# Optimization experiments

Measured on AMD Instinct MI355X. Metric: run time of the kernel, lower is better.

Reference implementation:

```python
import jax, jax.numpy as jnp
import numpy as np

THRESH = 0.5
MARGIN = 0.1
SCALE_POS = 2.0
SCALE_NEG = 50.0
EPS = 1e-5


def setup_inputs() -> dict:
    key = jax.random.key(0)
    k1, k2 = jax.random.split(key)
    B, D = 8192, 256
    feats = jax.random.normal(k1, (B, D), dtype=jnp.float32)
    # speaker embeddings are L2-normalized (cosine similarity, thresh=0.5 assumes this)
    feats = feats / jnp.linalg.norm(feats, axis=-1, keepdims=True)
    labels = jax.random.randint(k2, (B,), 0, 512, dtype=jnp.int64)
    return {"feats": feats, "labels": labels}


def reference(feats, labels):
    B = feats.shape[0]
    sim = jnp.matmul(feats, feats.T)                      # [B, B]
    same = labels[:, None] == labels[None, :]             # [B, B]

    pos_mask = same & (sim < 1.0 - EPS)                   # pos_pair_ (drops self-sim ~1)
    neg_mask = ~same                                      # neg_pair_

    neg_inf = jnp.float32(-jnp.inf)
    pos_inf = jnp.float32(jnp.inf)
    min_pos = jnp.min(jnp.where(pos_mask, sim, pos_inf), axis=1)  # min(pos_pair_)
    max_neg = jnp.max(jnp.where(neg_mask, sim, neg_inf), axis=1)  # max(neg_pair_)

    # dynamic re-masking (hard mining)
    neg_sel = neg_mask & (sim > (min_pos - MARGIN)[:, None])
    pos_sel = pos_mask & (sim < (max_neg + MARGIN)[:, None])

    valid = jnp.any(neg_sel, axis=1) & jnp.any(pos_sel, axis=1)

    # masked sums of exponentials via exp(-inf)=0; single fused mask+exp+sum
    pos_sum = jnp.sum(jnp.exp(jnp.where(pos_sel, -SCALE_POS * (sim - THRESH), neg_inf)), axis=1)
    neg_sum = jnp.sum(jnp.exp(jnp.where(neg_sel, SCALE_NEG * (sim - THRESH), neg_inf)), axis=1)

    row_loss = (1.0 / SCALE_POS) * jnp.log1p(pos_sum) + (1.0 / SCALE_NEG) * jnp.log1p(neg_sum)
    loss = jnp.sum(jnp.where(valid, row_loss, 0.0)) / B
    prec1 = jnp.mean(1.0 - valid.astype(jnp.float32))
    return loss, prec1
```

## Files before the change

kernel.cpp:

```cpp
#include <hip/hip_runtime.h>
#include <hip/hip_cooperative_groups.h>
#include <stdint.h>

namespace cg = cooperative_groups;


typedef __attribute__((ext_vector_type(8))) short short8;
typedef __attribute__((ext_vector_type(4))) float floatx4;

constexpr int D = 256;
constexpr int BM = 128;
constexpr int NT = 64;
constexpr int GPS = 8;
constexpr int NPB = NT * GPS;
constexpr int CPS = 33;
constexpr int BT = 512;
constexpr int CHUNK_SH = BM * 64;

__device__ __forceinline__ unsigned f2bf(float f) {
  unsigned u = __float_as_uint(f);
  return (u + 0x7FFFu + ((u >> 16) & 1u)) >> 16;
}

__device__ __forceinline__ void gl_lds16(const void* g, void* l) {
  __builtin_amdgcn_global_load_lds(
      (const __attribute__((address_space(1))) unsigned int*)g,
      (__attribute__((address_space(3))) unsigned int*)l, 16, 0, 0);
}

template <int PASS>
__device__ __forceinline__ void pair_body(
    int bid, const unsigned short* __restrict__ fb, const int* __restrict__ labels,
    const float* __restrict__ tmn, const float* __restrict__ tmx,
    float* __restrict__ rp0, float* __restrict__ rp1,
    float* __restrict__ cp0, float* __restrict__ cp1,
    short* As, short* Bs, int* labA, float* tA0, float* tA1) {
  const int I   = bid >> 3;
  const int g   = bid & 7;
  const int nT  = (I < 32) ? 33 : 32;
  const int t0  = (g * nT) >> 3;
  const int t1  = ((g + 1) * nT) >> 3;
  const int row0 = I * BM;

  const int tid  = threadIdx.x;
  const int lane = tid & 63;
  const int wave = tid >> 6;
  const int l15  = lane & 15;
  const int quad = lane >> 4;
  const int wr   = (wave >> 1) * 32;
  const int wc   = (wave & 1) * 64;

  const float ONE_EPS = 1.0f - 1e-5f;
  const float INF = __builtin_inff();

  __syncthreads();
  if (tid < BM) {
    labA[tid] = labels[row0 + tid];
    if (PASS == 2) { tA0[tid] = tmn[row0 + tid]; tA1[tid] = tmx[row0 + tid]; }
  }

  auto stage = [&](int b, int col0, int kc) {
#pragma unroll
    for (int j = 0; j < 2; ++j) {
      int idx = j * BT + tid;
      int r   = idx >> 3;
      int sl  = idx & 7;
      int cb  = sl ^ (r & 7);
      const char* ga = (const char*)fb + (((size_t)(row0 + r)) << 9) + (kc << 7) + (cb << 4);
      const char* gb = (const char*)fb + (((size_t)(col0 + r)) << 9) + (kc << 7) + (cb << 4);
      gl_lds16(ga, (char*)As + (size_t)b * (CHUNK_SH * 2) + ((size_t)idx << 4));
      gl_lds16(gb, (char*)Bs + (size_t)b * (CHUNK_SH * 2) + ((size_t)idx << 4));
    }
  };

  int arow[2], brow[4];
#pragma unroll
  for (int i = 0; i < 2; ++i) arow[i] = wr + i * 16 + l15;
#pragma unroll
  for (int i = 0; i < 4; ++i) brow[i] = wc + i * 16 + l15;

  float s0[8], s1[8];
#pragma unroll
  for (int i = 0; i < 8; ++i) {
    s0[i] = (PASS == 1) ? INF : 0.f;
    s1[i] = (PASS == 1) ? -INF : 0.f;
  }

  stage(0, ((I + t0) & 63) * BM, 0);

  int cur = 0;
  for (int off = t0; off < t1; ++off) {
    const int J = (I + off) & 63;
    const int col0 = J * BM;
    const bool diag = (off == 0);

    floatx4 acc[2][4];
#pragma unroll
    for (int rf = 0; rf < 2; ++rf)
#pragma unroll
      for (int cf = 0; cf < 4; ++cf)
        acc[rf][cf] = (floatx4)(0.f);

#pragma unroll
    for (int kc = 0; kc < 4; ++kc) {
      if (kc < 3) {
        stage(cur ^ 1, col0, kc + 1);
        asm volatile("s_waitcnt vmcnt(4)" ::: "memory");
      } else if (off + 1 < t1) {
        stage(cur ^ 1, ((I + off + 1) & 63) * BM, 0);
        asm volatile("s_waitcnt vmcnt(4)" ::: "memory");
      } else {
        asm volatile("s_waitcnt vmcnt(0)" ::: "memory");
      }
      __builtin_amdgcn_s_barrier();
      asm volatile("" ::: "memory");

      const short* Ab = As + cur * CHUNK_SH;
      const short* Bb = Bs + cur * CHUNK_SH;
#pragma unroll
      for (int ks = 0; ks < 2; ++ks) {
        const int gg = ks * 4 + quad;
        short8 a[2], b[4];
#pragma unroll
        for (int rf = 0; rf < 2; ++rf)
          a[rf] = *(const short8*)(Ab + arow[rf] * 64 + ((gg ^ (arow[rf] & 7)) << 3));
#pragma unroll
        for (int cf = 0; cf < 4; ++cf)
          b[cf] = *(const short8*)(Bb + brow[cf] * 64 + ((gg ^ (brow[cf] & 7)) << 3));
#pragma unroll
        for (int rf = 0; rf < 2; ++rf)
#pragma unroll
          for (int cf = 0; cf < 4; ++cf)
            acc[rf][cf] = __builtin_amdgcn_mfma_f32_16x16x32_bf16(a[rf], b[cf], acc[rf][cf], 0, 0, 0);
      }
      asm volatile("s_waitcnt lgkmcnt(0)" ::: "memory");
      __builtin_amdgcn_s_barrier();
      asm volatile("" ::: "memory");
      cur ^= 1;
    }

    int labc[4];
    float tBn[4], tBx[4];
#pragma unroll
    for (int cf = 0; cf < 4; ++cf) {
      int ci = col0 + wc + cf * 16 + l15;
      labc[cf] = labels[ci];
      if (PASS == 2) { tBn[cf] = tmn[ci]; tBx[cf] = tmx[ci]; }
    }

    float c0[4], c1[4];
#pragma unroll
    for (int i = 0; i < 4; ++i) {
      c0[i] = (PASS == 1) ? INF : 0.f;
      c1[i] = (PASS == 1) ? -INF : 0.f;
    }

#pragma unroll
    for (int rf = 0; rf < 2; ++rf) {
#pragma unroll
      for (int r = 0; r < 4; ++r) {
        const int ri = wr + rf * 16 + quad * 4 + r;
        const int lr = labA[ri];
        float tRn = 0.f, tRx = 0.f;
        if (PASS == 2) { tRn = tA0[ri]; tRx = tA1[ri]; }
#pragma unroll
        for (int cf = 0; cf < 4; ++cf) {
          float sim = acc[rf][cf][r];
          bool same = (lr == labc[cf]);
          bool posok = same && (sim < ONE_EPS);
          if (PASS == 1) {
            float pc = posok ? sim : INF;
            float nc = same ? -INF : sim;
            s0[rf * 4 + r] = fminf(s0[rf * 4 + r], pc);
            s1[rf * 4 + r] = fmaxf(s1[rf * 4 + r], nc);
            c0[cf] = fminf(c0[cf], pc);
            c1[cf] = fmaxf(c1[cf], nc);
          } else {
            if (posok) {
              float e = __expf(fmaf(-2.f, sim, 1.f));
              if (sim < tRx)      s0[rf * 4 + r] += e;
              if (sim < tBx[cf])  c0[cf] += e;
            } else if (!same) {
              float e = (sim > 0.22f) ? __expf(fmaf(50.f, sim, -25.f)) : 0.f;
              if (sim > tRn)      s1[rf * 4 + r] += 1e-30f + e;
              if (sim > tBn[cf])  c1[cf] += 1e-30f + e;
            }
          }
        }
      }
    }

    if (!diag) {
#pragma unroll
      for (int cf = 0; cf < 4; ++cf) {
        float v = c0[cf], w = c1[cf];
#pragma unroll
        for (int m = 16; m < 64; m <<= 1) {
          float vv = __shfl_xor(v, m), ww = __shfl_xor(w, m);
          v = (PASS == 1) ? fminf(v, vv) : (v + vv);
          w = (PASS == 1) ? fmaxf(w, ww) : (w + ww);
        }
        if (quad == 0) {
          size_t o = (size_t)(I * CPS + off) * 512 + (size_t)(wr >> 5) * 128 + wc + cf * 16 + l15;
          cp0[o] = v;
          cp1[o] = w;
        }
      }
    }
  }

#pragma unroll
  for (int i = 0; i < 8; ++i) {
#pragma unroll
    for (int m = 1; m < 16; m <<= 1) {
      float v = __shfl_xor(s0[i], m), w = __shfl_xor(s1[i], m);
      s0[i] = (PASS == 1) ? fminf(s0[i], v) : (s0[i] + v);
      s1[i] = (PASS == 1) ? fmaxf(s1[i], w) : (s1[i] + w);
    }
  }
  if (l15 == 0) {
#pragma unroll
    for (int rf = 0; rf < 2; ++rf)
#pragma unroll
      for (int r = 0; r < 4; ++r) {
        int ri = wr + rf * 16 + quad * 4 + r;
        size_t o = (size_t)bid * 256 + (size_t)(wc >> 6) * 128 + ri;
        rp0[o] = s0[rf * 4 + r];
        rp1[o] = s1[rf * 4 + r];
      }
  }
}

template <int PASS>
__device__ __forceinline__ void reduce_body(
    int T, const float* __restrict__ rp0, const float* __restrict__ rp1,
    const float* __restrict__ cp0, const float* __restrict__ cp1,
    float* __restrict__ o0, float* __restrict__ o1, float* __restrict__ out,
    float* sA, float* sB, float* sred) {
  const int q  = threadIdx.x & 127;
  const int h4 = threadIdx.x >> 7;

  float a = (PASS == 1) ? __builtin_inff() : 0.f;
  float b = (PASS == 1) ? -__builtin_inff() : 0.f;
#pragma unroll
  for (int g = 0; g < 4; ++g) {
    int c = h4 * 4 + g;
    int gg = c >> 1, half = c & 1;
    size_t o = (size_t)(T * GPS + gg) * 256 + (size_t)half * 128 + q;
    float v0 = rp0[o], v1 = rp1[o];
    a = (PASS == 1) ? fminf(a, v0) : (a + v0);
    b = (PASS == 1) ? fmaxf(b, v1) : (b + v1);
  }
#pragma unroll
  for (int off = 1; off <= 31; ++off) {
    int Is = (T - off) & 63;
    size_t o = (size_t)(Is * CPS + off) * 512 + (size_t)h4 * 128 + q;
    float v0 = cp0[o], v1 = cp1[o];
    a = (PASS == 1) ? fminf(a, v0) : (a + v0);
    b = (PASS == 1) ? fmaxf(b, v1) : (b + v1);
  }
  if (T >= 32) {
    int Is = T - 32;
    size_t o = (size_t)(Is * CPS + 32) * 512 + (size_t)h4 * 128 + q;
    float v0 = cp0[o], v1 = cp1[o];
    a = (PASS == 1) ? fminf(a, v0) : (a + v0);
    b = (PASS == 1) ? fmaxf(b, v1) : (b + v1);
  }
  if (h4 > 0) { sA[(h4 - 1) * 128 + q] = a; sB[(h4 - 1) * 128 + q] = b; }
  __syncthreads();
  if (h4 == 0) {
#pragma unroll
    for (int p = 0; p < 3; ++p) {
      float v0 = sA[p * 128 + q], v1 = sB[p * 128 + q];
      a = (PASS == 1) ? fminf(a, v0) : (a + v0);
      b = (PASS == 1) ? fmaxf(b, v1) : (b + v1);
    }
    if (PASS == 1) {
      o0[T * 128 + q] = a - 0.1f;
      o1[T * 128 + q] = b + 0.1f;
    } else {
      float loss = 0.f, cnt = 0.f;
      if (a > 0.f && b > 0.f) {
        loss = 0.5f * log1pf(a) + 0.02f * log1pf(b);
        cnt = 1.f;
      }
#pragma unroll
      for (int m = 1; m < 64; m <<= 1) {
        loss += __shfl_xor(loss, m);
        cnt  += __shfl_xor(cnt, m);
      }
      int wv = threadIdx.x >> 6, ln = threadIdx.x & 63;
      if (ln == 0) { sred[wv] = loss; sred[4 + wv] = cnt; }
    }
  }
  if (PASS == 2) {
    __syncthreads();
    if (threadIdx.x == 0) {
      float L = sred[0] + sred[1];
      float C = sred[4] + sred[5];
      atomicAdd(out, L / 8192.0f);
      atomicAdd(out + 1, -C / 8192.0f);
    }
  }
}

__global__ __launch_bounds__(BT, 4)
void mega_kernel(const float* feats, const int* labels, unsigned short* fb,
                 float* rp0, float* rp1, float* cp0, float* cp1,
                 float* tmn, float* tmx, float* out) {
  __shared__ __align__(16) short As[2 * CHUNK_SH];
  __shared__ __align__(16) short Bs[2 * CHUNK_SH];
  __shared__ int   labA[BM];
  __shared__ float tA0[BM], tA1[BM];

  cg::grid_group grid = cg::this_grid();
  const int bid = blockIdx.x;
  const int tid = threadIdx.x;

  const int n4 = 8192 * D / 4;
  for (int i = bid * BT + tid; i < n4; i += NPB * BT) {
    float4 v = ((const float4*)feats)[i];
    unsigned lo = f2bf(v.x) | (f2bf(v.y) << 16);
    unsigned hi = f2bf(v.z) | (f2bf(v.w) << 16);
    ((uint2*)fb)[i] = make_uint2(lo, hi);
  }
  if (bid == 0 && tid == 0) { out[0] = 0.f; out[1] = 1.f; }
  __threadfence();
  grid.sync();

  pair_body<1>(bid, fb, labels, nullptr, nullptr, rp0, rp1, cp0, cp1,
               As, Bs, labA, tA0, tA1);
  __threadfence();
  grid.sync();

  if (bid < NT)
    reduce_body<1>(bid, rp0, rp1, cp0, cp1, tmn, tmx, out,
                   (float*)As, (float*)As + 384, (float*)As + 768);
  __threadfence();
  grid.sync();

  pair_body<2>(bid, fb, labels, tmn, tmx, rp0, rp1, cp0, cp1,
               As, Bs, labA, tA0, tA1);
  __threadfence();
  grid.sync();

  if (bid < NT)
    reduce_body<2>(bid, rp0, rp1, cp0, cp1, nullptr, nullptr, out,
                   (float*)As, (float*)As + 384, (float*)As + 768);
}

__global__ void convert_kernel(const float* __restrict__ feats,
                               unsigned short* __restrict__ fb, int n4,
                               float* __restrict__ out) {
  int i = blockIdx.x * blockDim.x + threadIdx.x;
  if (i < n4) {
    float4 v = ((const float4*)feats)[i];
    unsigned lo = f2bf(v.x) | (f2bf(v.y) << 16);
    unsigned hi = f2bf(v.z) | (f2bf(v.w) << 16);
    ((uint2*)fb)[i] = make_uint2(lo, hi);
  }
  if (blockIdx.x == 0 && threadIdx.x == 0) { out[0] = 0.f; out[1] = 1.f; }
}

template <int PASS>
__global__ __launch_bounds__(BT, 4)
void pair_kernel(const unsigned short* __restrict__ fb, const int* __restrict__ labels,
                 const float* __restrict__ tmn, const float* __restrict__ tmx,
                 float* __restrict__ rp0, float* __restrict__ rp1,
                 float* __restrict__ cp0, float* __restrict__ cp1) {
  __shared__ __align__(16) short As[2 * CHUNK_SH];
  __shared__ __align__(16) short Bs[2 * CHUNK_SH];
  __shared__ int   labA[BM];
  __shared__ float tA0[BM], tA1[BM];
  pair_body<PASS>(blockIdx.x, fb, labels, tmn, tmx, rp0, rp1, cp0, cp1,
                  As, Bs, labA, tA0, tA1);
}

template <int PASS>
__global__ void reduce_kernel(const float* __restrict__ rp0, const float* __restrict__ rp1,
                              const float* __restrict__ cp0, const float* __restrict__ cp1,
                              float* __restrict__ o0, float* __restrict__ o1,
                              float* __restrict__ out) {
  __shared__ float sA[384], sB[384], sred[8];
  reduce_body<PASS>(blockIdx.x, rp0, rp1, cp0, cp1, o0, o1, out, sA, sB, sred);
}

extern "C" void kernel_launch(void* const* d_in, const int* in_sizes, int n_in,
                              void* d_out, int out_size, void* d_ws, size_t ws_size,
                              hipStream_t stream) {
  const float* feats  = (const float*)d_in[0];
  const int*   labels = (const int*)d_in[1];
  const int Bn = in_sizes[1];
  float* out = (float*)d_out;

  unsigned short* fb = (unsigned short*)d_ws;
  float* rp0 = (float*)((char*)d_ws + (size_t)Bn * D * 2);
  float* rp1 = rp0 + (size_t)NPB * 256;
  float* cp0 = rp1 + (size_t)NPB * 256;
  float* cp1 = cp0 + (size_t)NT * CPS * 512;
  float* tmn = cp1 + (size_t)NT * CPS * 512;
  float* tmx = tmn + Bn;

  bool launched = false;
  int maxb = 0;
  hipError_t qe = hipOccupancyMaxActiveBlocksPerMultiprocessor(
      &maxb, (const void*)mega_kernel, BT, 0);
  if (qe == hipSuccess && maxb * 256 >= NPB) {
    void* args[] = {(void*)&feats, (void*)&labels, (void*)&fb,
                    (void*)&rp0, (void*)&rp1, (void*)&cp0, (void*)&cp1,
                    (void*)&tmn, (void*)&tmx, (void*)&out};
    hipError_t le = hipLaunchCooperativeKernel(
        (const void*)mega_kernel, dim3(NPB), dim3(BT), args, 0, stream);
    launched = (le == hipSuccess);
  }
  if (!launched) {
    int n4 = Bn * D / 4;
    convert_kernel<<<(n4 + 255) / 256, 256, 0, stream>>>(feats, fb, n4, out);
    pair_kernel<1><<<NPB, BT, 0, stream>>>(fb, labels, nullptr, nullptr, rp0, rp1, cp0, cp1);
    reduce_kernel<1><<<NT, BT, 0, stream>>>(rp0, rp1, cp0, cp1, tmn, tmx, out);
    pair_kernel<2><<<NPB, BT, 0, stream>>>(fb, labels, tmn, tmx, rp0, rp1, cp0, cp1);
    reduce_kernel<2><<<NT, BT, 0, stream>>>(rp0, rp1, cp0, cp1, nullptr, nullptr, out);
  }
}
```

Before: 145.0 us.

## Cache pass-1 similarity tiles in workspace and reload them in pass 2

When the workspace is large enough, pass 1 writes each fp32 similarity tile to global memory with nontemporal stores. Pass 2 reloads these tiles instead of restaging bf16 features and recomputing the MFMA GEMM. This removes the second matrix multiply but adds a large write and read of the full similarity matrix through HBM. The path is selected at launch based on workspace size.

```diff
diff --git a/kernel.cpp b/kernel.cpp
--- a/kernel.cpp
+++ b/kernel.cpp
@@ -16,6 +16,8 @@
 constexpr int CPS = 33;
 constexpr int BT = 512;
 constexpr int CHUNK_SH = BM * 64;
+constexpr int TILE_SLOTS = NT * CPS;
+constexpr size_t TILE_V4 = 8 * BT;
 
 __device__ __forceinline__ unsigned f2bf(float f) {
   unsigned u = __float_as_uint(f);
@@ -28,13 +30,16 @@
       (__attribute__((address_space(3))) unsigned int*)l, 16, 0, 0);
 }
 
-template <int PASS>
+template <int PASS, bool CACHED>
 __device__ __forceinline__ void pair_body(
     int bid, const unsigned short* __restrict__ fb, const int* __restrict__ labels,
     const float* __restrict__ tmn, const float* __restrict__ tmx,
     float* __restrict__ rp0, float* __restrict__ rp1,
     float* __restrict__ cp0, float* __restrict__ cp1,
+    floatx4* __restrict__ simsv,
     short* As, short* Bs, int* labA, float* tA0, float* tA1) {
+  constexpr bool COMPUTE = (PASS == 1) || !CACHED;
+
   const int I   = bid >> 3;
   const int g   = bid & 7;
   const int nT  = (I < 32) ? 33 : 32;
@@ -57,6 +62,9 @@
   if (tid < BM) {
     labA[tid] = labels[row0 + tid];
     if (PASS == 2) { tA0[tid] = tmn[row0 + tid]; tA1[tid] = tmx[row0 + tid]; }
+  }
+  if constexpr (!COMPUTE) {
+    __syncthreads();
   }
 
   auto stage = [&](int b, int col0, int kc) {
@@ -86,7 +94,9 @@
     s1[i] = (PASS == 1) ? -INF : 0.f;
   }
 
-  stage(0, ((I + t0) & 63) * BM, 0);
+  if constexpr (COMPUTE) {
+    stage(0, ((I + t0) & 63) * BM, 0);
+  }
 
   int cur = 0;
   for (int off = t0; off < t1; ++off) {
@@ -94,51 +104,6 @@
     const int col0 = J * BM;
     const bool diag = (off == 0);
 
-    floatx4 acc[2][4];
-#pragma unroll
-    for (int rf = 0; rf < 2; ++rf)
-#pragma unroll
-      for (int cf = 0; cf < 4; ++cf)
-        acc[rf][cf] = (floatx4)(0.f);
-
-#pragma unroll
-    for (int kc = 0; kc < 4; ++kc) {
-      if (kc < 3) {
-        stage(cur ^ 1, col0, kc + 1);
-        asm volatile("s_waitcnt vmcnt(4)" ::: "memory");
-      } else if (off + 1 < t1) {
-        stage(cur ^ 1, ((I + off + 1) & 63) * BM, 0);
-        asm volatile("s_waitcnt vmcnt(4)" ::: "memory");
-      } else {
-        asm volatile("s_waitcnt vmcnt(0)" ::: "memory");
-      }
-      __builtin_amdgcn_s_barrier();
-      asm volatile("" ::: "memory");
-
-      const short* Ab = As + cur * CHUNK_SH;
-      const short* Bb = Bs + cur * CHUNK_SH;
-#pragma unroll
-      for (int ks = 0; ks < 2; ++ks) {
-        const int gg = ks * 4 + quad;
-        short8 a[2], b[4];
-#pragma unroll
-        for (int rf = 0; rf < 2; ++rf)
-          a[rf] = *(const short8*)(Ab + arow[rf] * 64 + ((gg ^ (arow[rf] & 7)) << 3));
-#pragma unroll
-        for (int cf = 0; cf < 4; ++cf)
-          b[cf] = *(const short8*)(Bb + brow[cf] * 64 + ((gg ^ (brow[cf] & 7)) << 3));
-#pragma unroll
-        for (int rf = 0; rf < 2; ++rf)
-#pragma unroll
-          for (int cf = 0; cf < 4; ++cf)
-            acc[rf][cf] = __builtin_amdgcn_mfma_f32_16x16x32_bf16(a[rf], b[cf], acc[rf][cf], 0, 0, 0);
-      }
-      asm volatile("s_waitcnt lgkmcnt(0)" ::: "memory");
-      __builtin_amdgcn_s_barrier();
-      asm volatile("" ::: "memory");
-      cur ^= 1;
-    }
-
     int labc[4];
     float tBn[4], tBx[4];
 #pragma unroll
@@ -146,6 +111,69 @@
       int ci = col0 + wc + cf * 16 + l15;
       labc[cf] = labels[ci];
       if (PASS == 2) { tBn[cf] = tmn[ci]; tBx[cf] = tmx[ci]; }
+    }
+
+    floatx4 acc[2][4];
+    if constexpr (COMPUTE) {
+#pragma unroll
+      for (int rf = 0; rf < 2; ++rf)
+#pragma unroll
+        for (int cf = 0; cf < 4; ++cf)
+          acc[rf][cf] = (floatx4)(0.f);
+
+#pragma unroll
+      for (int kc = 0; kc < 4; ++kc) {
+        if (kc < 3) {
+          stage(cur ^ 1, col0, kc + 1);
+          asm volatile("s_waitcnt vmcnt(4)" ::: "memory");
+        } else if (off + 1 < t1) {
+          stage(cur ^ 1, ((I + off + 1) & 63) * BM, 0);
+          asm volatile("s_waitcnt vmcnt(4)" ::: "memory");
+        } else {
+          asm volatile("s_waitcnt vmcnt(0)" ::: "memory");
+        }
+        __builtin_amdgcn_s_barrier();
+        asm volatile("" ::: "memory");
+
+        const short* Ab = As + cur * CHUNK_SH;
+        const short* Bb = Bs + cur * CHUNK_SH;
+#pragma unroll
+        for (int ks = 0; ks < 2; ++ks) {
+          const int gg = ks * 4 + quad;
+          short8 a[2], b[4];
+#pragma unroll
+          for (int rf = 0; rf < 2; ++rf)
+            a[rf] = *(const short8*)(Ab + arow[rf] * 64 + ((gg ^ (arow[rf] & 7)) << 3));
+#pragma unroll
+          for (int cf = 0; cf < 4; ++cf)
+            b[cf] = *(const short8*)(Bb + brow[cf] * 64 + ((gg ^ (brow[cf] & 7)) << 3));
+#pragma unroll
+          for (int rf = 0; rf < 2; ++rf)
+#pragma unroll
+            for (int cf = 0; cf < 4; ++cf)
+              acc[rf][cf] = __builtin_amdgcn_mfma_f32_16x16x32_bf16(a[rf], b[cf], acc[rf][cf], 0, 0, 0);
+        }
+        asm volatile("s_waitcnt lgkmcnt(0)" ::: "memory");
+        __builtin_amdgcn_s_barrier();
+        asm volatile("" ::: "memory");
+        cur ^= 1;
+      }
+    } else {
+      const floatx4* tp = simsv + (size_t)(I * CPS + off) * TILE_V4;
+#pragma unroll
+      for (int rf = 0; rf < 2; ++rf)
+#pragma unroll
+        for (int cf = 0; cf < 4; ++cf)
+          acc[rf][cf] = __builtin_nontemporal_load(tp + (size_t)(rf * 4 + cf) * BT + tid);
+    }
+
+    if constexpr (PASS == 1 && CACHED) {
+      floatx4* tp = simsv + (size_t)(I * CPS + off) * TILE_V4;
+#pragma unroll
+      for (int rf = 0; rf < 2; ++rf)
+#pragma unroll
+        for (int cf = 0; cf < 4; ++cf)
+          __builtin_nontemporal_store(acc[rf][cf], tp + (size_t)(rf * 4 + cf) * BT + tid);
     }
 
     float c0[4], c1[4];
@@ -304,10 +332,11 @@
   }
 }
 
+template <int CACHED>
 __global__ __launch_bounds__(BT, 4)
 void mega_kernel(const float* feats, const int* labels, unsigned short* fb,
                  float* rp0, float* rp1, float* cp0, float* cp1,
-                 float* tmn, float* tmx, float* out) {
+                 float* tmn, float* tmx, floatx4* simsv, float* out) {
   __shared__ __align__(16) short As[2 * CHUNK_SH];
   __shared__ __align__(16) short Bs[2 * CHUNK_SH];
   __shared__ int   labA[BM];
@@ -328,8 +357,9 @@
   __threadfence();
   grid.sync();
 
-  pair_body<1>(bid, fb, labels, nullptr, nullptr, rp0, rp1, cp0, cp1,
-               As, Bs, labA, tA0, tA1);
+  pair_body<1, (bool)CACHED>(bid, fb, labels, nullptr, nullptr,
+                             rp0, rp1, cp0, cp1, simsv,
+                             As, Bs, labA, tA0, tA1);
   __threadfence();
   grid.sync();
 
@@ -339,8 +369,9 @@
   __threadfence();
   grid.sync();
 
-  pair_body<2>(bid, fb, labels, tmn, tmx, rp0, rp1, cp0, cp1,
-               As, Bs, labA, tA0, tA1);
+  pair_body<2, (bool)CACHED>(bid, fb, labels, tmn, tmx,
+                             rp0, rp1, cp0, cp1, simsv,
+                             As, Bs, labA, tA0, tA1);
   __threadfence();
   grid.sync();
 
@@ -372,8 +403,8 @@
   __shared__ __align__(16) short Bs[2 * CHUNK_SH];
   __shared__ int   labA[BM];
   __shared__ float tA0[BM], tA1[BM];
-  pair_body<PASS>(blockIdx.x, fb, labels, tmn, tmx, rp0, rp1, cp0, cp1,
-                  As, Bs, labA, tA0, tA1);
+  pair_body<PASS, false>(blockIdx.x, fb, labels, tmn, tmx, rp0, rp1, cp0, cp1,
+                         nullptr, As, Bs, labA, tA0, tA1);
 }
 
 template <int PASS>
@@ -393,24 +424,28 @@
   const int Bn = in_sizes[1];
   float* out = (float*)d_out;
 
-  unsigned short* fb = (unsigned short*)d_ws;
-  float* rp0 = (float*)((char*)d_ws + (size_t)Bn * D * 2);
-  float* rp1 = rp0 + (size_t)NPB * 256;
-  float* cp0 = rp1 + (size_t)NPB * 256;
-  float* cp1 = cp0 + (size_t)NT * CPS * 512;
-  float* tmn = cp1 + (size_t)NT * CPS * 512;
-  float* tmx = tmn + Bn;
+  char* base = (char*)d_ws;
+  unsigned short* fb = (unsigned short*)base;
+  size_t o = (size_t)Bn * D * 2;
+  float* rp0 = (float*)(base + o);  o += (size_t)NPB * 256 * 4;
+  float* rp1 = (float*)(base + o);  o += (size_t)NPB * 256 * 4;
+  float* cp0 = (float*)(base + o);  o += (size_t)NT * CPS * 512 * 4;
+  float* cp1 = (float*)(base + o);  o += (size_t)NT * CPS * 512 * 4;
+  float* tmn = (float*)(base + o);  o += (size_t)Bn * 4;
+  float* tmx = (float*)(base + o);  o += (size_t)Bn * 4;
+  floatx4* simsv = (floatx4*)(base + o);
+  size_t need = o + (size_t)TILE_SLOTS * TILE_V4 * 16;
+  const int cached = (ws_size >= need) ? 1 : 0;
 
   bool launched = false;
   int maxb = 0;
-  hipError_t qe = hipOccupancyMaxActiveBlocksPerMultiprocessor(
-      &maxb, (const void*)mega_kernel, BT, 0);
+  const void* kfn = cached ? (const void*)mega_kernel<1> : (const void*)mega_kernel<0>;
+  hipError_t qe = hipOccupancyMaxActiveBlocksPerMultiprocessor(&maxb, kfn, BT, 0);
   if (qe == hipSuccess && maxb * 256 >= NPB) {
     void* args[] = {(void*)&feats, (void*)&labels, (void*)&fb,
                     (void*)&rp0, (void*)&rp1, (void*)&cp0, (void*)&cp1,
-                    (void*)&tmn, (void*)&tmx, (void*)&out};
-    hipError_t le = hipLaunchCooperativeKernel(
-        (const void*)mega_kernel, dim3(NPB), dim3(BT), args, 0, stream);
+                    (void*)&tmn, (void*)&tmx, (void*)&simsv, (void*)&out};
+    hipError_t le = hipLaunchCooperativeKernel(kfn, dim3(NPB), dim3(BT), args, 0, stream);
     launched = (le == hipSuccess);
   }
   if (!launched) {
```

After: 140.4 us. 3.2% less time.

## Replace second similarity GEMM pass with sparse candidate-pair records and atomic apply

Applied to the files above, without the earlier changes.

The first pair pass now also writes out the sparse set of candidate pairs: positives, plus negatives whose similarity exceeds 0.22. Each record carries the pair's indices and similarity and goes into a fixed-capacity buffer per block. A cheap apply phase then uses the mined thresholds and atomics to add the exponentials into per-row accumulators. This removes the second full bf16 GEMM recompute. The validity test is rewritten to compare the row extrema directly with the thresholds, and a label histogram stands in for the epsilon per-negative term. The costs are a shared-memory atomic inside the hot epilogue, global atomics during apply, and a per-block cap of 2048 records that assumes candidate pairs are sparse; excess records would be silently dropped.

```diff
diff --git a/kernel.cpp b/kernel.cpp
--- a/kernel.cpp
+++ b/kernel.cpp
@@ -16,6 +16,7 @@
 constexpr int CPS = 33;
 constexpr int BT = 512;
 constexpr int CHUNK_SH = BM * 64;
+constexpr int RECCAP = 2048;
 
 __device__ __forceinline__ unsigned f2bf(float f) {
   unsigned u = __float_as_uint(f);
@@ -28,13 +29,12 @@
       (__attribute__((address_space(3))) unsigned int*)l, 16, 0, 0);
 }
 
-template <int PASS>
-__device__ __forceinline__ void pair_body(
+__device__ __forceinline__ void pair1_body(
     int bid, const unsigned short* __restrict__ fb, const int* __restrict__ labels,
-    const float* __restrict__ tmn, const float* __restrict__ tmx,
     float* __restrict__ rp0, float* __restrict__ rp1,
     float* __restrict__ cp0, float* __restrict__ cp1,
-    short* As, short* Bs, int* labA, float* tA0, float* tA1) {
+    uint2* __restrict__ recs, int* __restrict__ reccnt,
+    short* As, short* Bs, int* labA, int* emitCnt) {
   const int I   = bid >> 3;
   const int g   = bid & 7;
   const int nT  = (I < 32) ? 33 : 32;
@@ -53,11 +53,9 @@
   const float ONE_EPS = 1.0f - 1e-5f;
   const float INF = __builtin_inff();
 
+  if (tid == 0) *emitCnt = 0;
   __syncthreads();
-  if (tid < BM) {
-    labA[tid] = labels[row0 + tid];
-    if (PASS == 2) { tA0[tid] = tmn[row0 + tid]; tA1[tid] = tmx[row0 + tid]; }
-  }
+  if (tid < BM) labA[tid] = labels[row0 + tid];
 
   auto stage = [&](int b, int col0, int kc) {
 #pragma unroll
@@ -81,10 +79,7 @@
 
   float s0[8], s1[8];
 #pragma unroll
-  for (int i = 0; i < 8; ++i) {
-    s0[i] = (PASS == 1) ? INF : 0.f;
-    s1[i] = (PASS == 1) ? -INF : 0.f;
-  }
+  for (int i = 0; i < 8; ++i) { s0[i] = INF; s1[i] = -INF; }
 
   stage(0, ((I + t0) & 63) * BM, 0);
 
@@ -93,6 +88,14 @@
     const int J = (I + off) & 63;
     const int col0 = J * BM;
     const bool diag = (off == 0);
+
+    int labc[4], cidx[4];
+#pragma unroll
+    for (int cf = 0; cf < 4; ++cf) {
+      int ci = col0 + wc + cf * 16 + l15;
+      cidx[cf] = ci;
+      labc[cf] = labels[ci];
+    }
 
     floatx4 acc[2][4];
 #pragma unroll
@@ -139,21 +142,9 @@
       cur ^= 1;
     }
 
-    int labc[4];
-    float tBn[4], tBx[4];
-#pragma unroll
-    for (int cf = 0; cf < 4; ++cf) {
-      int ci = col0 + wc + cf * 16 + l15;
-      labc[cf] = labels[ci];
-      if (PASS == 2) { tBn[cf] = tmn[ci]; tBx[cf] = tmx[ci]; }
-    }
-
     float c0[4], c1[4];
 #pragma unroll
-    for (int i = 0; i < 4; ++i) {
-      c0[i] = (PASS == 1) ? INF : 0.f;
-      c1[i] = (PASS == 1) ? -INF : 0.f;
-    }
+    for (int i = 0; i < 4; ++i) { c0[i] = INF; c1[i] = -INF; }
 
 #pragma unroll
     for (int rf = 0; rf < 2; ++rf) {
@@ -161,30 +152,24 @@
       for (int r = 0; r < 4; ++r) {
         const int ri = wr + rf * 16 + quad * 4 + r;
         const int lr = labA[ri];
-        float tRn = 0.f, tRx = 0.f;
-        if (PASS == 2) { tRn = tA0[ri]; tRx = tA1[ri]; }
 #pragma unroll
         for (int cf = 0; cf < 4; ++cf) {
           float sim = acc[rf][cf][r];
           bool same = (lr == labc[cf]);
           bool posok = same && (sim < ONE_EPS);
-          if (PASS == 1) {
-            float pc = posok ? sim : INF;
-            float nc = same ? -INF : sim;
-            s0[rf * 4 + r] = fminf(s0[rf * 4 + r], pc);
-            s1[rf * 4 + r] = fmaxf(s1[rf * 4 + r], nc);
-            c0[cf] = fminf(c0[cf], pc);
-            c1[cf] = fmaxf(c1[cf], nc);
-          } else {
-            if (posok) {
-              float e = __expf(fmaf(-2.f, sim, 1.f));
-              if (sim < tRx)      s0[rf * 4 + r] += e;
-              if (sim < tBx[cf])  c0[cf] += e;
-            } else if (!same) {
-              float e = (sim > 0.22f) ? __expf(fmaf(50.f, sim, -25.f)) : 0.f;
-              if (sim > tRn)      s1[rf * 4 + r] += 1e-30f + e;
-              if (sim > tBn[cf])  c1[cf] += 1e-30f + e;
-            }
+          float pc = posok ? sim : INF;
+          float nc = same ? -INF : sim;
+          s0[rf * 4 + r] = fminf(s0[rf * 4 + r], pc);
+          s1[rf * 4 + r] = fmaxf(s1[rf * 4 + r], nc);
+          c0[cf] = fminf(c0[cf], pc);
+          c1[cf] = fmaxf(c1[cf], nc);
+          bool hotn = (!same) && (sim > 0.22f);
+          if (posok || hotn) {
+            unsigned key = (unsigned)(row0 + ri) | ((unsigned)cidx[cf] << 13) |
+                           (diag ? (1u << 26) : 0u) | (hotn ? (1u << 27) : 0u);
+            int slot = atomicAdd(emitCnt, 1);
+            if (slot < RECCAP)
+              recs[(size_t)bid * RECCAP + slot] = make_uint2(key, __float_as_uint(sim));
           }
         }
       }
@@ -197,8 +182,8 @@
 #pragma unroll
         for (int m = 16; m < 64; m <<= 1) {
           float vv = __shfl_xor(v, m), ww = __shfl_xor(w, m);
-          v = (PASS == 1) ? fminf(v, vv) : (v + vv);
-          w = (PASS == 1) ? fmaxf(w, ww) : (w + ww);
+          v = fminf(v, vv);
+          w = fmaxf(w, ww);
         }
         if (quad == 0) {
           size_t o = (size_t)(I * CPS + off) * 512 + (size_t)(wr >> 5) * 128 + wc + cf * 16 + l15;
@@ -214,8 +199,8 @@
 #pragma unroll
     for (int m = 1; m < 16; m <<= 1) {
       float v = __shfl_xor(s0[i], m), w = __shfl_xor(s1[i], m);
-      s0[i] = (PASS == 1) ? fminf(s0[i], v) : (s0[i] + v);
-      s1[i] = (PASS == 1) ? fmaxf(s1[i], w) : (s1[i] + w);
+      s0[i] = fminf(s0[i], v);
+      s1[i] = fmaxf(s1[i], w);
     }
   }
   if (l15 == 0) {
@@ -229,89 +214,126 @@
         rp1[o] = s1[rf * 4 + r];
       }
   }
-}
-
-template <int PASS>
-__device__ __forceinline__ void reduce_body(
+  __syncthreads();
+  if (tid == 0) reccnt[bid] = (*emitCnt < RECCAP) ? *emitCnt : RECCAP;
+}
+
+__device__ __forceinline__ void reduce1_body(
     int T, const float* __restrict__ rp0, const float* __restrict__ rp1,
     const float* __restrict__ cp0, const float* __restrict__ cp1,
-    float* __restrict__ o0, float* __restrict__ o1, float* __restrict__ out,
-    float* sA, float* sB, float* sred) {
+    float* __restrict__ o0, float* __restrict__ o1,
+    float* __restrict__ mpv, float* __restrict__ mnv,
+    float* sA, float* sB) {
   const int q  = threadIdx.x & 127;
   const int h4 = threadIdx.x >> 7;
 
-  float a = (PASS == 1) ? __builtin_inff() : 0.f;
-  float b = (PASS == 1) ? -__builtin_inff() : 0.f;
+  float a = __builtin_inff();
+  float b = -__builtin_inff();
 #pragma unroll
   for (int g = 0; g < 4; ++g) {
     int c = h4 * 4 + g;
     int gg = c >> 1, half = c & 1;
     size_t o = (size_t)(T * GPS + gg) * 256 + (size_t)half * 128 + q;
-    float v0 = rp0[o], v1 = rp1[o];
-    a = (PASS == 1) ? fminf(a, v0) : (a + v0);
-    b = (PASS == 1) ? fmaxf(b, v1) : (b + v1);
+    a = fminf(a, rp0[o]);
+    b = fmaxf(b, rp1[o]);
   }
 #pragma unroll
   for (int off = 1; off <= 31; ++off) {
     int Is = (T - off) & 63;
     size_t o = (size_t)(Is * CPS + off) * 512 + (size_t)h4 * 128 + q;
-    float v0 = cp0[o], v1 = cp1[o];
-    a = (PASS == 1) ? fminf(a, v0) : (a + v0);
-    b = (PASS == 1) ? fmaxf(b, v1) : (b + v1);
+    a = fminf(a, cp0[o]);
+    b = fmaxf(b, cp1[o]);
   }
   if (T >= 32) {
     int Is = T - 32;
     size_t o = (size_t)(Is * CPS + 32) * 512 + (size_t)h4 * 128 + q;
-    float v0 = cp0[o], v1 = cp1[o];
-    a = (PASS == 1) ? fminf(a, v0) : (a + v0);
-    b = (PASS == 1) ? fmaxf(b, v1) : (b + v1);
+    a = fminf(a, cp0[o]);
+    b = fmaxf(b, cp1[o]);
   }
   if (h4 > 0) { sA[(h4 - 1) * 128 + q] = a; sB[(h4 - 1) * 128 + q] = b; }
   __syncthreads();
   if (h4 == 0) {
 #pragma unroll
     for (int p = 0; p < 3; ++p) {
-      float v0 = sA[p * 128 + q], v1 = sB[p * 128 + q];
-      a = (PASS == 1) ? fminf(a, v0) : (a + v0);
-      b = (PASS == 1) ? fmaxf(b, v1) : (b + v1);
-    }
-    if (PASS == 1) {
-      o0[T * 128 + q] = a - 0.1f;
-      o1[T * 128 + q] = b + 0.1f;
+      a = fminf(a, sA[p * 128 + q]);
+      b = fmaxf(b, sB[p * 128 + q]);
+    }
+    o0[T * 128 + q]  = a - 0.1f;
+    o1[T * 128 + q]  = b + 0.1f;
+    mpv[T * 128 + q] = a;
+    mnv[T * 128 + q] = b;
+  }
+}
+
+__device__ __forceinline__ void apply_body(
+    int bid, const uint2* __restrict__ recs, const int* __restrict__ reccnt,
+    const float* __restrict__ tmn, const float* __restrict__ tmx,
+    float* __restrict__ pos_acc, float* __restrict__ neg_acc) {
+  const int cnt = reccnt[bid];
+  for (int k = threadIdx.x; k < cnt; k += BT) {
+    uint2 rec = recs[(size_t)bid * RECCAP + k];
+    int ri = rec.x & 8191;
+    int ci = (rec.x >> 13) & 8191;
+    bool dg = (rec.x >> 26) & 1;
+    bool ng = (rec.x >> 27) & 1;
+    float sim = __uint_as_float(rec.y);
+    if (!ng) {
+      float e = __expf(fmaf(-2.f, sim, 1.f));
+      if (sim < tmx[ri])        atomicAdd(&pos_acc[ri], e);
+      if (!dg && sim < tmx[ci]) atomicAdd(&pos_acc[ci], e);
     } else {
-      float loss = 0.f, cnt = 0.f;
-      if (a > 0.f && b > 0.f) {
-        loss = 0.5f * log1pf(a) + 0.02f * log1pf(b);
-        cnt = 1.f;
-      }
-#pragma unroll
-      for (int m = 1; m < 64; m <<= 1) {
-        loss += __shfl_xor(loss, m);
-        cnt  += __shfl_xor(cnt, m);
-      }
-      int wv = threadIdx.x >> 6, ln = threadIdx.x & 63;
-      if (ln == 0) { sred[wv] = loss; sred[4 + wv] = cnt; }
-    }
-  }
-  if (PASS == 2) {
-    __syncthreads();
-    if (threadIdx.x == 0) {
-      float L = sred[0] + sred[1];
-      float C = sred[4] + sred[5];
-      atomicAdd(out, L / 8192.0f);
-      atomicAdd(out + 1, -C / 8192.0f);
-    }
+      float e = __expf(fmaf(50.f, sim, -25.f));
+      if (sim > tmn[ri])        atomicAdd(&neg_acc[ri], e);
+      if (!dg && sim > tmn[ci]) atomicAdd(&neg_acc[ci], e);
+    }
+  }
+}
+
+__device__ __forceinline__ void final_body(
+    int T, const int* __restrict__ labels, const int* __restrict__ labcnt,
+    const float* __restrict__ pos_acc, const float* __restrict__ neg_acc,
+    const float* __restrict__ tmn, const float* __restrict__ tmx,
+    const float* __restrict__ mpv, const float* __restrict__ mnv,
+    float* __restrict__ out, float* sred) {
+  const int tid = threadIdx.x;
+  float loss = 0.f, cval = 0.f;
+  if (tid < 128) {
+    int r = T * 128 + tid;
+    float a = pos_acc[r];
+    float b = neg_acc[r] + (float)(8192 - labcnt[labels[r]]) * 1e-30f;
+    bool valid = (mnv[r] > tmn[r]) && (mpv[r] < tmx[r]);
+    if (valid) {
+      loss = 0.5f * log1pf(a) + 0.02f * log1pf(b);
+      cval = 1.f;
+    }
+  }
+#pragma unroll
+  for (int m = 1; m < 64; m <<= 1) {
+    loss += __shfl_xor(loss, m);
+    cval += __shfl_xor(cval, m);
+  }
+  int wv = tid >> 6, ln = tid & 63;
+  if (ln == 0) { sred[wv] = loss; sred[8 + wv] = cval; }
+  __syncthreads();
+  if (tid == 0) {
+    float L = 0.f, C = 0.f;
+#pragma unroll
+    for (int w = 0; w < 8; ++w) { L += sred[w]; C += sred[8 + w]; }
+    atomicAdd(out, L / 8192.0f);
+    atomicAdd(out + 1, -C / 8192.0f);
   }
 }
 
 __global__ __launch_bounds__(BT, 4)
 void mega_kernel(const float* feats, const int* labels, unsigned short* fb,
                  float* rp0, float* rp1, float* cp0, float* cp1,
-                 float* tmn, float* tmx, float* out) {
+                 float* tmn, float* tmx, float* mpv, float* mnv,
+                 float* pos_acc, float* neg_acc, int* labcnt,
+                 uint2* recs, int* reccnt, float* out) {
   __shared__ __align__(16) short As[2 * CHUNK_SH];
   __shared__ __align__(16) short Bs[2 * CHUNK_SH];
-  __shared__ int   labA[BM];
-  __shared__ float tA0[BM], tA1[BM];
+  __shared__ int labA[BM];
+  __shared__ int emitCnt;
 
   cg::grid_group grid = cg::this_grid();
   const int bid = blockIdx.x;
@@ -324,34 +346,42 @@
     unsigned hi = f2bf(v.z) | (f2bf(v.w) << 16);
     ((uint2*)fb)[i] = make_uint2(lo, hi);
   }
+  for (int i = bid * BT + tid; i < 8192; i += NPB * BT) {
+    pos_acc[i] = 0.f;
+    neg_acc[i] = 0.f;
+  }
+  if (bid == 0 && tid < 512) labcnt[tid] = 0;
   if (bid == 0 && tid == 0) { out[0] = 0.f; out[1] = 1.f; }
   __threadfence();
   grid.sync();
 
-  pair_body<1>(bid, fb, labels, nullptr, nullptr, rp0, rp1, cp0, cp1,
-               As, Bs, labA, tA0, tA1);
+  pair1_body(bid, fb, labels, rp0, rp1, cp0, cp1, recs, reccnt,
+             As, Bs, labA, &emitCnt);
   __threadfence();
   grid.sync();
 
-  if (bid < NT)
-    reduce_body<1>(bid, rp0, rp1, cp0, cp1, tmn, tmx, out,
-                   (float*)As, (float*)As + 384, (float*)As + 768);
+  if (bid < NT) {
+    reduce1_body(bid, rp0, rp1, cp0, cp1, tmn, tmx, mpv, mnv,
+                 (float*)As, (float*)As + 384);
+  } else if (bid < NT + 16) {
+    for (int i = (bid - NT) * BT + tid; i < 8192; i += 16 * BT)
+      atomicAdd(&labcnt[labels[i]], 1);
+  }
   __threadfence();
   grid.sync();
 
-  pair_body<2>(bid, fb, labels, tmn, tmx, rp0, rp1, cp0, cp1,
-               As, Bs, labA, tA0, tA1);
+  apply_body(bid, recs, reccnt, tmn, tmx, pos_acc, neg_acc);
   __threadfence();
   grid.sync();
 
   if (bid < NT)
-    reduce_body<2>(bid, rp0, rp1, cp0, cp1, nullptr, nullptr, out,
-                   (float*)As, (float*)As + 384, (float*)As + 768);
-}
-
-__global__ void convert_kernel(const float* __restrict__ feats,
-                               unsigned short* __restrict__ fb, int n4,
-                               float* __restrict__ out) {
+    final_body(bid, labels, labcnt, pos_acc, neg_acc, tmn, tmx, mpv, mnv,
+               out, (float*)As);
+}
+
+__global__ void k_convert(const float* __restrict__ feats, unsigned short* __restrict__ fb,
+                          float* __restrict__ pos_acc, float* __restrict__ neg_acc,
+                          int* __restrict__ labcnt, float* __restrict__ out, int n4) {
   int i = blockIdx.x * blockDim.x + threadIdx.x;
   if (i < n4) {
     float4 v = ((const float4*)feats)[i];
@@ -359,30 +389,51 @@
     unsigned hi = f2bf(v.z) | (f2bf(v.w) << 16);
     ((uint2*)fb)[i] = make_uint2(lo, hi);
   }
-  if (blockIdx.x == 0 && threadIdx.x == 0) { out[0] = 0.f; out[1] = 1.f; }
-}
-
-template <int PASS>
+  if (i < 8192) { pos_acc[i] = 0.f; neg_acc[i] = 0.f; }
+  if (i < 512) labcnt[i] = 0;
+  if (i == 0) { out[0] = 0.f; out[1] = 1.f; }
+}
+
 __global__ __launch_bounds__(BT, 4)
-void pair_kernel(const unsigned short* __restrict__ fb, const int* __restrict__ labels,
-                 const float* __restrict__ tmn, const float* __restrict__ tmx,
-                 float* __restrict__ rp0, float* __restrict__ rp1,
-                 float* __restrict__ cp0, float* __restrict__ cp1) {
+void k_pair1(const unsigned short* __restrict__ fb, const int* __restrict__ labels,
+             float* __restrict__ rp0, float* __restrict__ rp1,
+             float* __restrict__ cp0, float* __restrict__ cp1,
+             uint2* __restrict__ recs, int* __restrict__ reccnt) {
   __shared__ __align__(16) short As[2 * CHUNK_SH];
   __shared__ __align__(16) short Bs[2 * CHUNK_SH];
-  __shared__ int   labA[BM];
-  __shared__ float tA0[BM], tA1[BM];
-  pair_body<PASS>(blockIdx.x, fb, labels, tmn, tmx, rp0, rp1, cp0, cp1,
-                  As, Bs, labA, tA0, tA1);
-}
-
-template <int PASS>
-__global__ void reduce_kernel(const float* __restrict__ rp0, const float* __restrict__ rp1,
-                              const float* __restrict__ cp0, const float* __restrict__ cp1,
-                              float* __restrict__ o0, float* __restrict__ o1,
-                              float* __restrict__ out) {
-  __shared__ float sA[384], sB[384], sred[8];
-  reduce_body<PASS>(blockIdx.x, rp0, rp1, cp0, cp1, o0, o1, out, sA, sB, sred);
+  __shared__ int labA[BM];
+  __shared__ int emitCnt;
+  pair1_body(blockIdx.x, fb, labels, rp0, rp1, cp0, cp1, recs, reccnt,
+             As, Bs, labA, &emitCnt);
+}
+
+__global__ void k_reduce1(const float* __restrict__ rp0, const float* __restrict__ rp1,
+                          const float* __restrict__ cp0, const float* __restrict__ cp1,
+                          float* __restrict__ tmn, float* __restrict__ tmx,
+                          float* __restrict__ mpv, float* __restrict__ mnv) {
+  __shared__ float sA[384], sB[384];
+  reduce1_body(blockIdx.x, rp0, rp1, cp0, cp1, tmn, tmx, mpv, mnv, sA, sB);
+}
+
+__global__ void k_hist(const int* __restrict__ labels, int* __restrict__ labcnt) {
+  int i = blockIdx.x * blockDim.x + threadIdx.x;
+  if (i < 8192) atomicAdd(&labcnt[labels[i]], 1);
+}
+
+__global__ void k_apply(const uint2* __restrict__ recs, const int* __restrict__ reccnt,
+                        const float* __restrict__ tmn, const float* __restrict__ tmx,
+                        float* __restrict__ pos_acc, float* __restrict__ neg_acc) {
+  apply_body(blockIdx.x, recs, reccnt, tmn, tmx, pos_acc, neg_acc);
+}
+
+__global__ void k_final(const int* __restrict__ labels, const int* __restrict__ labcnt,
+                        const float* __restrict__ pos_acc, const float* __restrict__ neg_acc,
+                        const float* __restrict__ tmn, const float* __restrict__ tmx,
+                        const float* __restrict__ mpv, const float* __restrict__ mnv,
+                        float* __restrict__ out) {
+  __shared__ float sred[16];
+  final_body(blockIdx.x, labels, labcnt, pos_acc, neg_acc, tmn, tmx, mpv, mnv,
+             out, sred);
 }
 
 extern "C" void kernel_launch(void* const* d_in, const int* in_sizes, int n_in,
@@ -393,13 +444,22 @@
   const int Bn = in_sizes[1];
   float* out = (float*)d_out;
 
-  unsigned short* fb = (unsigned short*)d_ws;
-  float* rp0 = (float*)((char*)d_ws + (size_t)Bn * D * 2);
-  float* rp1 = rp0 + (size_t)NPB * 256;
-  float* cp0 = rp1 + (size_t)NPB * 256;
-  float* cp1 = cp0 + (size_t)NT * CPS * 512;
-  float* tmn = cp1 + (size_t)NT * CPS * 512;
-  float* tmx = tmn + Bn;
+  char* base = (char*)d_ws;
+  unsigned short* fb = (unsigned short*)base;
+  size_t o = (size_t)Bn * D * 2;
+  float* rp0 = (float*)(base + o);  o += (size_t)NPB * 256 * 4;
+  float* rp1 = (float*)(base + o);  o += (size_t)NPB * 256 * 4;
+  float* cp0 = (float*)(base + o);  o += (size_t)NT * CPS * 512 * 4;
+  float* cp1 = (float*)(base + o);  o += (size_t)NT * CPS * 512 * 4;
+  uint2* recs = (uint2*)(base + o); o += (size_t)NPB * RECCAP * 8;
+  float* tmn = (float*)(base + o);  o += (size_t)Bn * 4;
+  float* tmx = (float*)(base + o);  o += (size_t)Bn * 4;
+  float* mpv = (float*)(base + o);  o += (size_t)Bn * 4;
+  float* mnv = (float*)(base + o);  o += (size_t)Bn * 4;
+  float* pos_acc = (float*)(base + o); o += (size_t)Bn * 4;
+  float* neg_acc = (float*)(base + o); o += (size_t)Bn * 4;
+  int* labcnt = (int*)(base + o);   o += 512 * 4;
+  int* reccnt = (int*)(base + o);   o += (size_t)NPB * 4;
 
   bool launched = false;
   int maxb = 0;
@@ -408,17 +468,20 @@
   if (qe == hipSuccess && maxb * 256 >= NPB) {
     void* args[] = {(void*)&feats, (void*)&labels, (void*)&fb,
                     (void*)&rp0, (void*)&rp1, (void*)&cp0, (void*)&cp1,
-                    (void*)&tmn, (void*)&tmx, (void*)&out};
+                    (void*)&tmn, (void*)&tmx, (void*)&mpv, (void*)&mnv,
+                    (void*)&pos_acc, (void*)&neg_acc, (void*)&labcnt,
+                    (void*)&recs, (void*)&reccnt, (void*)&out};
     hipError_t le = hipLaunchCooperativeKernel(
         (const void*)mega_kernel, dim3(NPB), dim3(BT), args, 0, stream);
     launched = (le == hipSuccess);
   }
   if (!launched) {
     int n4 = Bn * D / 4;
-    convert_kernel<<<(n4 + 255) / 256, 256, 0, stream>>>(feats, fb, n4, out);
-    pair_kernel<1><<<NPB, BT, 0, stream>>>(fb, labels, nullptr, nullptr, rp0, rp1, cp0, cp1);
-    reduce_kernel<1><<<NT, BT, 0, stream>>>(rp0, rp1, cp0, cp1, tmn, tmx, out);
-    pair_kernel<2><<<NPB, BT, 0, stream>>>(fb, labels, tmn, tmx, rp0, rp1, cp0, cp1);
-    reduce_kernel<2><<<NT, BT, 0, stream>>>(rp0, rp1, cp0, cp1, nullptr, nullptr, out);
-  }
-}
+    k_convert<<<(n4 + 255) / 256, 256, 0, stream>>>(feats, fb, pos_acc, neg_acc, labcnt, out, n4);
+    k_pair1<<<NPB, BT, 0, stream>>>(fb, labels, rp0, rp1, cp0, cp1, recs, reccnt);
+    k_reduce1<<<NT, BT, 0, stream>>>(rp0, rp1, cp0, cp1, tmn, tmx, mpv, mnv);
+    k_hist<<<16, BT, 0, stream>>>(labels, labcnt);
+    k_apply<<<NPB, BT, 0, stream>>>(recs, reccnt, tmn, tmx, pos_acc, neg_acc);
+    k_final<<<NT, BT, 0, stream>>>(labels, labcnt, pos_acc, neg_acc, tmn, tmx, mpv, mnv, out);
+  }
+}
```

Measured after the change: 132.3 us. -8.8%, faster.
